# Kernel tuning notes

Measured on AMD Instinct MI355X. Metric: run time of the kernel, lower is better.

The kernel has to match this reference:

```python
import jax, jax.numpy as jnp
import numpy as np

N_BINS = 15


def setup_inputs() -> dict:
    key = jax.random.key(0)
    k1, k2 = jax.random.split(key)
    N, C = 2097152, 100
    logits = jax.random.normal(k1, (N, C), dtype=jnp.float32)
    labels = jax.random.randint(k2, (N,), 0, C, dtype=jnp.int64)
    return {"logits": logits, "labels": labels}


def reference(logits, labels):
    # softmax probabilities, top-1 confidence and prediction
    softmaxes = jax.nn.softmax(logits, axis=-1)          # [N, C]
    confidences = jnp.max(softmaxes, axis=1)             # [N]
    predictions = jnp.argmax(softmaxes, axis=1)          # [N]
    accuracies = (predictions == labels).astype(logits.dtype)

    n = logits.shape[0]
    # Torch bins are (i/n_bins, (i+1)/n_bins]; ceil(c*n_bins)-1 maps c into bin i.
    # confidences >= 1/C > 0, so every sample lands in some bin.
    bin_idx = jnp.clip(jnp.ceil(confidences * N_BINS).astype(jnp.int32) - 1, 0, N_BINS - 1)

    ones = jnp.ones_like(confidences)
    counts = jax.ops.segment_sum(ones, bin_idx, num_segments=N_BINS)         # [B]
    conf_sums = jax.ops.segment_sum(confidences, bin_idx, num_segments=N_BINS)
    acc_sums = jax.ops.segment_sum(accuracies, bin_idx, num_segments=N_BINS)

    prop_in_bin = counts / n
    safe_counts = jnp.maximum(counts, 1.0)
    gap = jnp.abs(conf_sums / safe_counts - acc_sums / safe_counts)
    ece = jnp.sum(jnp.where(counts > 0, gap * prop_in_bin, 0.0))
    return ece.reshape(1)
```

## Files before the change

### kernel.cpp

```cpp
#include <hip/hip_runtime.h>

typedef float f32x4 __attribute__((ext_vector_type(4)));

#define N_BINS 15
#define NCLASS 100
#define ROWS_PER_BLOCK 64

__global__ __launch_bounds__(256) void ece_pass1(
    const float* __restrict__ logits,
    const int* __restrict__ labels,
    float* __restrict__ bins,
    int n_rows)
{
    __shared__ float priv[ROWS_PER_BLOCK * 45];
    const int tid = threadIdx.x;
    for (int k = tid; k < ROWS_PER_BLOCK * 45; k += 256) priv[k] = 0.f;
    __syncthreads();

    const int q    = tid & 3;
    const int slot = tid >> 2;
    const int stride = gridDim.x * ROWS_PER_BLOCK;
    float* pb = &priv[slot * 45];

    for (int row = blockIdx.x * ROWS_PER_BLOCK + slot; row < n_rows;
         row += stride) {
        const float* rp = logits + (size_t)row * NCLASS;
        const f32x4* rv = (const f32x4*)rp;

        f32x4 F[6];
        #pragma unroll
        for (int i = 0; i < 6; ++i) F[i] = rv[q + 4 * i];

        f32x4 T = { -1e30f, -1e30f, -1e30f, -1e30f };
        if (q == 0) T = rv[24];

        int lab = 0;
        if (q == 0) lab = labels[row];

        f32x4 m4 = F[0];
        f32x4 s4;
        s4.x = __expf(F[0].x); s4.y = __expf(F[0].y);
        s4.z = __expf(F[0].z); s4.w = __expf(F[0].w);
        #pragma unroll
        for (int i = 1; i < 6; ++i) {
            m4.x = fmaxf(m4.x, F[i].x); m4.y = fmaxf(m4.y, F[i].y);
            m4.z = fmaxf(m4.z, F[i].z); m4.w = fmaxf(m4.w, F[i].w);
            s4.x += __expf(F[i].x); s4.y += __expf(F[i].y);
            s4.z += __expf(F[i].z); s4.w += __expf(F[i].w);
        }
        m4.x = fmaxf(m4.x, T.x); m4.y = fmaxf(m4.y, T.y);
        m4.z = fmaxf(m4.z, T.z); m4.w = fmaxf(m4.w, T.w);
        s4.x += __expf(T.x); s4.y += __expf(T.y);
        s4.z += __expf(T.z); s4.w += __expf(T.w);

        float vm = fmaxf(fmaxf(m4.x, m4.y), fmaxf(m4.z, m4.w));
        float ss = (s4.x + s4.y) + (s4.z + s4.w);

        float pv = 0.f;
        if (q == 0) pv = rp[lab];

        #pragma unroll
        for (int off = 1; off <= 2; off <<= 1) {
            ss += __shfl_xor(ss, off, 4);
            vm = fmaxf(vm, __shfl_xor(vm, off, 4));
        }

        if (q == 0) {
            float conf = __expf(vm) / ss;
            int b = (int)ceilf(conf * (float)N_BINS) - 1;
            b = min(max(b, 0), N_BINS - 1);
            pb[b]      += 1.0f;
            pb[15 + b] += conf;
            pb[30 + b] += (pv == vm) ? 1.0f : 0.0f;
        }
    }

    __syncthreads();
    if (tid < 45) {
        float v = 0.f;
        #pragma unroll 8
        for (int s = 0; s < ROWS_PER_BLOCK; ++s)
            v += priv[s * 45 + tid];
        atomicAdd(&bins[tid], v);
    }
}

__global__ void ece_final(const float* __restrict__ bins,
                          float* __restrict__ out, float n)
{
    if (threadIdx.x == 0) {
        float ece = 0.f;
        for (int i = 0; i < N_BINS; ++i) {
            float cnt = bins[i];
            if (cnt > 0.f) {
                float sc  = fmaxf(cnt, 1.0f);
                float gap = fabsf(bins[15 + i] / sc - bins[30 + i] / sc);
                ece += gap * (cnt / n);
            }
        }
        out[0] = ece;
    }
}

extern "C" void kernel_launch(void* const* d_in, const int* in_sizes, int n_in,
                              void* d_out, int out_size, void* d_ws, size_t ws_size,
                              hipStream_t stream)
{
    const float* logits = (const float*)d_in[0];
    const int*   labels = (const int*)d_in[1];
    float* out  = (float*)d_out;
    float* bins = (float*)d_ws;

    const int n_rows = in_sizes[1];

    hipMemsetAsync(bins, 0, 45 * sizeof(float), stream);

    ece_pass1<<<2048, 256, 0, stream>>>(logits, labels, bins, n_rows);
    ece_final<<<1, 64, 0, stream>>>(bins, out, (float)n_rows);
}
```

Baseline: 163.9 us.

## Double-buffer logits rows into LDS via direct global-to-LDS async loads

Stages 64 rows per block into a double-buffered LDS tile using global_load_lds, prefetching the next tile while the current one is processed. This replaces per-thread strided global reads with fully coalesced contiguous loads. The grid drops to a fixed 768 blocks, and the per-slot histogram shrinks to a single 45-entry LDS array updated with shared atomics. It adds a barrier per iteration and uses about 51KB of LDS per block, which limits occupancy. The LDS atomics may also contend.

Result: no change. 160.8 us, median of 2 (-1.9%).

```diff
diff --git a/kernel.cpp b/kernel.cpp
--- a/kernel.cpp
+++ b/kernel.cpp
@@ -2,30 +2,69 @@
 
 typedef float f32x4 __attribute__((ext_vector_type(4)));
 
+typedef __attribute__((address_space(1))) const void global_cv;
+typedef __attribute__((address_space(3))) void lds_v;
+
 #define N_BINS 15
 #define NCLASS 100
-#define ROWS_PER_BLOCK 64
+#define ROWS   64
+#define GRID   768
 
 __global__ __launch_bounds__(256) void ece_pass1(
     const float* __restrict__ logits,
     const int* __restrict__ labels,
     float* __restrict__ bins,
-    int n_rows)
+    int n_rows, int niter)
 {
-    __shared__ float priv[ROWS_PER_BLOCK * 45];
-    const int tid = threadIdx.x;
-    for (int k = tid; k < ROWS_PER_BLOCK * 45; k += 256) priv[k] = 0.f;
-    __syncthreads();
+    __shared__ __align__(16) float stage[2][ROWS * NCLASS];
+    __shared__ float priv[45];
 
+    const int tid  = threadIdx.x;
+    const int wave = tid >> 6;
     const int q    = tid & 3;
     const int slot = tid >> 2;
-    const int stride = gridDim.x * ROWS_PER_BLOCK;
-    float* pb = &priv[slot * 45];
 
-    for (int row = blockIdx.x * ROWS_PER_BLOCK + slot; row < n_rows;
-         row += stride) {
-        const float* rp = logits + (size_t)row * NCLASS;
+    if (tid < 45) priv[tid] = 0.f;
+
+    const long max_slot = (long)n_rows * (NCLASS / 4) - 1;
+    const f32x4* gv = (const f32x4*)logits;
+
+    auto issue_stage = [&](int buf, long row0) {
+        if (row0 >= n_rows) return;
+        const long s0 = row0 * (NCLASS / 4);
+        #pragma unroll
+        for (int r = 0; r < 6; ++r) {
+            long si = s0 + r * 256 + tid;
+            if (si > max_slot) si = max_slot;
+            __builtin_amdgcn_global_load_lds(
+                (global_cv*)(gv + si),
+                (lds_v*)&stage[buf][(r * 256 + wave * 64) * 4],
+                16, 0, 0);
+        }
+        if (wave == 0) {
+            long si = s0 + 1536 + tid;
+            if (si > max_slot) si = max_slot;
+            __builtin_amdgcn_global_load_lds(
+                (global_cv*)(gv + si),
+                (lds_v*)&stage[buf][1536 * 4],
+                16, 0, 0);
+        }
+    };
+
+    issue_stage(0, (long)blockIdx.x * ROWS);
+
+    for (int g = 0; g < niter; ++g) {
+        __syncthreads();
+        if (g + 1 < niter)
+            issue_stage((g + 1) & 1,
+                        ((long)(g + 1) * gridDim.x + blockIdx.x) * ROWS);
+
+        const long row = ((long)g * gridDim.x + blockIdx.x) * ROWS + slot;
+        const float* rp = &stage[g & 1][slot * NCLASS];
         const f32x4* rv = (const f32x4*)rp;
+
+        int lab = 0;
+        if (q == 0 && row < n_rows) lab = labels[row];
 
         f32x4 F[6];
         #pragma unroll
@@ -33,9 +72,6 @@
 
         f32x4 T = { -1e30f, -1e30f, -1e30f, -1e30f };
         if (q == 0) T = rv[24];
-
-        int lab = 0;
-        if (q == 0) lab = labels[row];
 
         f32x4 m4 = F[0];
         f32x4 s4;
@@ -65,24 +101,18 @@
             vm = fmaxf(vm, __shfl_xor(vm, off, 4));
         }
 
-        if (q == 0) {
+        if (q == 0 && row < n_rows) {
             float conf = __expf(vm) / ss;
             int b = (int)ceilf(conf * (float)N_BINS) - 1;
             b = min(max(b, 0), N_BINS - 1);
-            pb[b]      += 1.0f;
-            pb[15 + b] += conf;
-            pb[30 + b] += (pv == vm) ? 1.0f : 0.0f;
+            atomicAdd(&priv[b],      1.0f);
+            atomicAdd(&priv[15 + b], conf);
+            atomicAdd(&priv[30 + b], (pv == vm) ? 1.0f : 0.0f);
         }
     }
 
     __syncthreads();
-    if (tid < 45) {
-        float v = 0.f;
-        #pragma unroll 8
-        for (int s = 0; s < ROWS_PER_BLOCK; ++s)
-            v += priv[s * 45 + tid];
-        atomicAdd(&bins[tid], v);
-    }
+    if (tid < 45) atomicAdd(&bins[tid], priv[tid]);
 }
 
 __global__ void ece_final(const float* __restrict__ bins,
@@ -112,9 +142,10 @@
     float* bins = (float*)d_ws;
 
     const int n_rows = in_sizes[1];
+    const int rows_per_sweep = GRID * ROWS;
+    const int niter = (n_rows + rows_per_sweep - 1) / rows_per_sweep;
 
     hipMemsetAsync(bins, 0, 45 * sizeof(float), stream);
-
-    ece_pass1<<<2048, 256, 0, stream>>>(logits, labels, bins, n_rows);
+    ece_pass1<<<GRID, 256, 0, stream>>>(logits, labels, bins, n_rows, niter);
     ece_final<<<1, 64, 0, stream>>>(bins, out, (float)n_rows);
 }
```
